# Kernel optimization log

Measured on AMD Instinct MI355X. Metric: run time of the kernel, lower is better.

The kernel has to match this reference:

```python
import jax, jax.numpy as jnp
import numpy as np

D_MODEL = 1024
D_STATE = 16
D_CONV = 4
EXPAND = 2
D_INNER = EXPAND * D_MODEL          # 2048
DT_RANK = (D_MODEL + 15) // 16      # 64
B_SZ, L = 2, 2048


def setup_inputs() -> dict:
    key = jax.random.key(0)
    ks = jax.random.split(key, 14)
    s = 0.02
    dt_init = jax.random.uniform(ks[10], (D_INNER,), minval=1e-3, maxval=0.1)
    A = jnp.tile(jnp.arange(1, D_STATE + 1, dtype=jnp.float32)[None, :], (D_INNER, 1))
    return {
        "x_f": jax.random.normal(ks[0], (B_SZ, L, D_MODEL), jnp.float32),
        "x_h": jax.random.normal(ks[1], (B_SZ, L, D_MODEL), jnp.float32),
        "W_hf": s * jax.random.normal(ks[2], (D_MODEL, D_MODEL), jnp.float32),
        "b_hf": jnp.zeros((D_MODEL,), jnp.float32),
        "W_in": s * jax.random.normal(ks[3], (2 * D_INNER, D_MODEL), jnp.float32),
        "conv_w": s * jax.random.normal(ks[4], (D_INNER, 1, D_CONV), jnp.float32),
        "conv_b": jnp.zeros((D_INNER,), jnp.float32),
        "W_x": s * jax.random.normal(ks[5], (DT_RANK + 2 * D_STATE, D_INNER), jnp.float32),
        "W_dt": (DT_RANK ** -0.5) * jax.random.normal(ks[6], (D_INNER, DT_RANK), jnp.float32),
        "b_dt": jnp.log(jnp.expm1(dt_init)),
        "A_log": jnp.log(A),
        "D": jnp.ones((D_INNER,), jnp.float32),
        "W_out": s * jax.random.normal(ks[7], (D_MODEL, D_INNER), jnp.float32),
    }


def _mamba(x, W_in, conv_w, conv_b, W_x, W_dt, b_dt, A_log, D, W_out):
    B, Lx, _ = x.shape
    # in_proj -> x, z branches  [B, L, 2*d_inner]
    xz = jnp.einsum("bld,ed->ble", x, W_in)
    x_in, z = jnp.split(xz, 2, axis=-1)
    # causal depthwise conv1d, kernel d_conv, groups = d_inner
    x_nch = jnp.transpose(x_in, (0, 2, 1))  # [B, d_inner, L]
    x_conv = jax.lax.conv_general_dilated(
        x_nch, conv_w, window_strides=(1,), padding=[(D_CONV - 1, 0)],
        dimension_numbers=("NCH", "OIH", "NCH"), feature_group_count=D_INNER)
    x_c = jax.nn.silu(jnp.transpose(x_conv, (0, 2, 1)) + conv_b)  # [B, L, d_inner]
    # input-dependent dt, B, C
    x_dbl = jnp.einsum("ble,fe->blf", x_c, W_x)
    dt_r = x_dbl[..., :DT_RANK]
    B_ssm = x_dbl[..., DT_RANK:DT_RANK + D_STATE]          # [B, L, d_state]
    C_ssm = x_dbl[..., DT_RANK + D_STATE:]                  # [B, L, d_state]
    dt = jax.nn.softplus(jnp.einsum("blr,er->ble", dt_r, W_dt) + b_dt)  # [B, L, d_inner]
    A = -jnp.exp(A_log)  # [d_inner, d_state]

    # selective scan over time; carry h: [B, d_inner, d_state]
    def step(h, inp):
        dt_t, B_t, C_t, x_t = inp  # [B,d_inner], [B,d_state], [B,d_state], [B,d_inner]
        dA = jnp.exp(dt_t[:, :, None] * A)                       # [B, d_inner, d_state]
        dBx = dt_t[:, :, None] * B_t[:, None, :] * x_t[:, :, None]
        h = dA * h + dBx
        y_t = jnp.einsum("bes,bs->be", h, C_t)
        return h, y_t

    seq = (jnp.transpose(dt, (1, 0, 2)), jnp.transpose(B_ssm, (1, 0, 2)),
           jnp.transpose(C_ssm, (1, 0, 2)), jnp.transpose(x_c, (1, 0, 2)))
    h0 = jnp.zeros((B, D_INNER, D_STATE), x.dtype)
    _, ys = jax.lax.scan(step, h0, seq)
    y = jnp.transpose(ys, (1, 0, 2)) + D * x_c   # skip term
    y = y * jax.nn.silu(z)                        # output gate
    return jnp.einsum("ble,de->bld", y, W_out)


def reference(x_f, x_h, W_hf, b_hf, W_in, conv_w, conv_b, W_x, W_dt, b_dt, A_log, D, W_out):
    hf_gate = jax.nn.sigmoid(jnp.einsum("bld,ed->ble", x_h, W_hf) + b_hf)
    modulated = x_f * hf_gate
    return _mamba(modulated, W_in, conv_w, conv_b, W_x, W_dt, b_dt, A_log, D, W_out)
```

## Files before the change

### kernel.cpp

```cpp
#include <hip/hip_runtime.h>
#include <hip/hip_bf16.h>
#include <math.h>

#define L_SEQ  2048
#define BATCH  2
#define DMODEL 1024
#define DINNER 2048
#define DSTATE 16
#define NCHUNK 64
#define LCH    (L_SEQ / NCHUNK)

typedef __attribute__((ext_vector_type(8))) short bf16x8;
typedef __attribute__((ext_vector_type(4))) float f32x4;

__device__ __forceinline__ unsigned short f2bu(float x) {
    __hip_bfloat16 h = __float2bfloat16(x);
    return __builtin_bit_cast(unsigned short, h);
}
__device__ __forceinline__ float bu2f(unsigned short u) {
    __hip_bfloat16 h = __builtin_bit_cast(__hip_bfloat16, u);
    return __bfloat162float(h);
}
__device__ __forceinline__ float fast_exp2(float x) {
    float r; asm("v_exp_f32 %0, %1" : "=v"(r) : "v"(x)); return r;
}
#define LOG2E 1.44269504088896f

__global__ __launch_bounds__(256) void cvt_all(
    const float* __restrict__ Wout, const float* __restrict__ Win,
    const float* __restrict__ xh,   const float* __restrict__ Whf,
    const float* __restrict__ Wx,   const float* __restrict__ Wdt,
    __hip_bfloat16* __restrict__ dWout, __hip_bfloat16* __restrict__ dWin,
    __hip_bfloat16* __restrict__ dxh,   __hip_bfloat16* __restrict__ dWhf,
    __hip_bfloat16* __restrict__ dWx,   __hip_bfloat16* __restrict__ dWdt)
{
    int bid = blockIdx.x;
    const float* s; __hip_bfloat16* d;
    if (bid < 2048)       { s = Wout; d = dWout; }
    else if (bid < 6144)  { s = Win;  d = dWin;  bid -= 2048; }
    else if (bid < 10240) { s = xh;   d = dxh;   bid -= 6144; }
    else if (bid < 11264) { s = Whf;  d = dWhf;  bid -= 10240; }
    else if (bid < 11520) {
        bid -= 11264;
        const int i = (bid * 256 + threadIdx.x) * 4;
        const int r = i >> 11;
        ushort4 u = {0, 0, 0, 0};
        if (r < 96) {
            const float4 v = *reinterpret_cast<const float4*>(&Wx[i]);
            u.x = f2bu(v.x); u.y = f2bu(v.y); u.z = f2bu(v.z); u.w = f2bu(v.w);
        }
        *reinterpret_cast<ushort4*>(&dWx[i]) = u;
        return;
    }
    else                  { s = Wdt;  d = dWdt;  bid -= 11520; }
    const int i = (bid * 256 + threadIdx.x) * 4;
    const float4 v = *reinterpret_cast<const float4*>(&s[i]);
    ushort4 u;
    u.x = f2bu(v.x); u.y = f2bu(v.y); u.z = f2bu(v.z); u.w = f2bu(v.w);
    *reinterpret_cast<ushort4*>(&d[i]) = u;
}

__global__ __launch_bounds__(512) void mfma_gemm256(
    const __hip_bfloat16* __restrict__ A,
    const __hip_bfloat16* __restrict__ Bw,
    __hip_bfloat16* __restrict__ Cb,
    __hip_bfloat16* __restrict__ Cb2)
{
    __shared__ unsigned short As[2][256 * 64];
    __shared__ unsigned short Bs[2][256 * 64];
    const int tid = threadIdx.x;
    const int row0 = blockIdx.y * 256;
    const int col0 = blockIdx.x * 256;
    const int wid = tid >> 6, lane = tid & 63;
    const int wr = wid >> 2, wc = wid & 3;
    const int fr = lane & 15, fq = lane >> 4;

    f32x4 acc[8][4];
#pragma unroll
    for (int m = 0; m < 8; m++)
#pragma unroll
        for (int n = 0; n < 4; n++) acc[m][n] = (f32x4){0.f, 0.f, 0.f, 0.f};

    size_t gA[4], gB[4];
    int ld0[4];
#pragma unroll
    for (int l = 0; l < 4; l++) {
        const int item = l * 512 + tid;
        const int r = item >> 3, sl = item & 7;
        gA[l] = (size_t)(row0 + r) * 1024 + sl * 8;
        gB[l] = (size_t)(col0 + r) * 1024 + sl * 8;
        ld0[l] = item * 8;
    }

#if __has_builtin(__builtin_amdgcn_global_load_lds)
    auto STAGE = [&](int buf, int koff) {
#pragma unroll
        for (int l = 0; l < 4; l++)
            __builtin_amdgcn_global_load_lds(
                (const __attribute__((address_space(1))) unsigned int*)(A + gA[l] + koff),
                (__attribute__((address_space(3))) unsigned int*)&As[buf][ld0[l]], 16, 0, 0);
#pragma unroll
        for (int l = 0; l < 4; l++)
            __builtin_amdgcn_global_load_lds(
                (const __attribute__((address_space(1))) unsigned int*)(Bw + gB[l] + koff),
                (__attribute__((address_space(3))) unsigned int*)&Bs[buf][ld0[l]], 16, 0, 0);
    };
#else
    auto STAGE = [&](int buf, int koff) {
#pragma unroll
        for (int l = 0; l < 4; l++) {
            *reinterpret_cast<uint4*>(&As[buf][ld0[l]]) =
                *reinterpret_cast<const uint4*>(A + gA[l] + koff);
            *reinterpret_cast<uint4*>(&Bs[buf][ld0[l]]) =
                *reinterpret_cast<const uint4*>(Bw + gB[l] + koff);
        }
    };
#endif

    STAGE(0, 0);
    __syncthreads();
    int buf = 0;
    for (int t = 0; t < 16; t++) {
        if (t + 1 < 16) STAGE(buf ^ 1, (t + 1) * 64);
#pragma unroll
        for (int ks = 0; ks < 2; ks++) {
            bf16x8 a[8], b[4];
#pragma unroll
            for (int m = 0; m < 8; m++)
                a[m] = *reinterpret_cast<const bf16x8*>(
                    &As[buf][(wr * 128 + m * 16 + fr) * 64 + ks * 32 + fq * 8]);
#pragma unroll
            for (int n = 0; n < 4; n++)
                b[n] = *reinterpret_cast<const bf16x8*>(
                    &Bs[buf][(wc * 64 + n * 16 + fr) * 64 + ks * 32 + fq * 8]);
#pragma unroll
            for (int m = 0; m < 8; m++)
#pragma unroll
                for (int n = 0; n < 4; n++)
                    acc[m][n] = __builtin_amdgcn_mfma_f32_16x16x32_bf16(
                        a[m], b[n], acc[m][n], 0, 0, 0);
        }
        __syncthreads();
        buf ^= 1;
    }

    const int r0 = row0 + wr * 128;
    const int c0 = col0 + wc * 64;
    const bool isx = (col0 < 2048);
#pragma unroll
    for (int m = 0; m < 8; m++)
#pragma unroll
        for (int n = 0; n < 4; n++) {
            const int col = c0 + n * 16 + fr;
#pragma unroll
            for (int j = 0; j < 4; j++) {
                const int row = r0 + m * 16 + fq * 4 + j;
                const __hip_bfloat16 v = __float2bfloat16(acc[m][n][j]);
                if (isx) Cb[(size_t)row * 2048 + col] = v;
                else     Cb2[(size_t)row * 2048 + col - 2048] = v;
            }
        }
}

template <int EPI>
__global__ __launch_bounds__(256) void mfma_gemm(
    const __hip_bfloat16* __restrict__ A, int lda,
    const __hip_bfloat16* __restrict__ Bw, int ldb,
    int ksz,
    float* __restrict__ Cf, int ldc,
    __hip_bfloat16* __restrict__ Cb,
    const float* __restrict__ bias,
    const float* __restrict__ mul, int ldmul)
{
    __shared__ unsigned short As[128 * 32];
    __shared__ unsigned short Bs[128 * 32];
    const int tid = threadIdx.x;
    const int row0 = blockIdx.y * 128;
    const int col0 = blockIdx.x * 128;
    const int wid = tid >> 6, lane = tid & 63;
    const int wr = wid >> 1, wc = wid & 1;
    const int fr = lane & 15, fq = lane >> 4;
    const int kz0 = blockIdx.z * ksz;

    f32x4 acc[4][4];
#pragma unroll
    for (int i = 0; i < 4; i++)
#pragma unroll
        for (int j = 0; j < 4; j++) acc[i][j] = (f32x4){0.f, 0.f, 0.f, 0.f};

    const int i0 = tid, i1 = tid + 256;
    const size_t ga0 = (size_t)(row0 + (i0 >> 2)) * lda + (i0 & 3) * 8;
    const size_t ga1 = (size_t)(row0 + (i1 >> 2)) * lda + (i1 & 3) * 8;
    const size_t gb0 = (size_t)(col0 + (i0 >> 2)) * ldb + (i0 & 3) * 8;
    const size_t gb1 = (size_t)(col0 + (i1 >> 2)) * ldb + (i1 & 3) * 8;
    const int nk = ksz >> 5;

    for (int kk = 0; kk < nk; kk++) {
        const int koff = kz0 + kk * 32;
#if __has_builtin(__builtin_amdgcn_global_load_lds)
        __syncthreads();
        __builtin_amdgcn_global_load_lds(
            (const __attribute__((address_space(1))) unsigned int*)(A + ga0 + koff),
            (__attribute__((address_space(3))) unsigned int*)&As[i0 * 8], 16, 0, 0);
        __builtin_amdgcn_global_load_lds(
            (const __attribute__((address_space(1))) unsigned int*)(A + ga1 + koff),
            (__attribute__((address_space(3))) unsigned int*)&As[i1 * 8], 16, 0, 0);
        __builtin_amdgcn_global_load_lds(
            (const __attribute__((address_space(1))) unsigned int*)(Bw + gb0 + koff),
            (__attribute__((address_space(3))) unsigned int*)&Bs[i0 * 8], 16, 0, 0);
        __builtin_amdgcn_global_load_lds(
            (const __attribute__((address_space(1))) unsigned int*)(Bw + gb1 + koff),
            (__attribute__((address_space(3))) unsigned int*)&Bs[i1 * 8], 16, 0, 0);
        __syncthreads();
#else
        const uint4 va0 = *reinterpret_cast<const uint4*>(A + ga0 + koff);
        const uint4 va1 = *reinterpret_cast<const uint4*>(A + ga1 + koff);
        const uint4 vb0 = *reinterpret_cast<const uint4*>(Bw + gb0 + koff);
        const uint4 vb1 = *reinterpret_cast<const uint4*>(Bw + gb1 + koff);
        __syncthreads();
        *reinterpret_cast<uint4*>(&As[i0 * 8]) = va0;
        *reinterpret_cast<uint4*>(&As[i1 * 8]) = va1;
        *reinterpret_cast<uint4*>(&Bs[i0 * 8]) = vb0;
        *reinterpret_cast<uint4*>(&Bs[i1 * 8]) = vb1;
        __syncthreads();
#endif
        bf16x8 af[4], bq[4];
#pragma unroll
        for (int rb = 0; rb < 4; rb++)
            af[rb] = *reinterpret_cast<const bf16x8*>(
                &As[(wr * 64 + rb * 16 + fr) * 32 + fq * 8]);
#pragma unroll
        for (int cb = 0; cb < 4; cb++)
            bq[cb] = *reinterpret_cast<const bf16x8*>(
                &Bs[(wc * 64 + cb * 16 + fr) * 32 + fq * 8]);
#pragma unroll
        for (int rb = 0; rb < 4; rb++)
#pragma unroll
            for (int cb = 0; cb < 4; cb++)
                acc[rb][cb] = __builtin_amdgcn_mfma_f32_16x16x32_bf16(
                    af[rb], bq[cb], acc[rb][cb], 0, 0, 0);
    }

    float* Cz = Cf;
    if (EPI == 0)
        Cz = Cf + (size_t)blockIdx.z * (size_t)(gridDim.y * 128) * ldc;
    const int r0 = row0 + wr * 64, c0 = col0 + wc * 64;
#pragma unroll
    for (int rb = 0; rb < 4; rb++)
#pragma unroll
        for (int cb = 0; cb < 4; cb++) {
            const int col = c0 + cb * 16 + fr;
#pragma unroll
            for (int j = 0; j < 4; j++) {
                const int row = r0 + rb * 16 + fq * 4 + j;
                float v = acc[rb][cb][j];
                if (EPI == 0) {
                    Cz[(size_t)row * ldc + col] = v;
                } else if (EPI == 1) {
                    v = 1.f / (1.f + __expf(-(v + bias[col])));
                    v *= mul[(size_t)row * ldmul + col];
                    Cb[(size_t)row * ldc + col] = __float2bfloat16(v);
                } else {
                    v += bias[col];
                    v = (v > 20.f) ? v : log1pf(__expf(v));
                    Cb[(size_t)row * ldc + col] = __float2bfloat16(v);
                }
            }
        }
}

__global__ __launch_bounds__(256) void reduce_xdbl(
    const float* __restrict__ part, float* __restrict__ xdbl,
    __hip_bfloat16* __restrict__ dtr)
{
    const int i = blockIdx.x * 256 + threadIdx.x;
    float s = 0.f;
#pragma unroll
    for (int j = 0; j < 8; j++) s += part[(size_t)j * 524288 + i];
    xdbl[i] = s;
    const int col = i & 127;
    if (col < 64) dtr[((i >> 7) << 6) + col] = __float2bfloat16(s);
}

__global__ __launch_bounds__(256) void conv_silu_kernel(
    const __hip_bfloat16* __restrict__ xin_b, const float* __restrict__ cw,
    const float* __restrict__ cb, __hip_bfloat16* __restrict__ xcb)
{
    int gid = blockIdx.x * 256 + threadIdx.x;
    int e = gid & (DINNER - 1);
    int row = gid >> 11;
    int t = row & (L_SEQ - 1);
    float s = cb[e];
#pragma unroll
    for (int j = 0; j < 4; j++) {
        int tt = t - 3 + j;
        if (tt >= 0)
            s = fmaf(cw[e * 4 + j],
                     __bfloat162float(xin_b[(size_t)(row - 3 + j) * 2048 + e]), s);
    }
    xcb[(size_t)row * 2048 + e] = __float2bfloat16(s / (1.f + __expf(-s)));
}

__global__ __launch_bounds__(256) void scan_pass_a(
    const __hip_bfloat16* __restrict__ dtb, const __hip_bfloat16* __restrict__ xcb,
    const float* __restrict__ xdbl, const float* __restrict__ A_log,
    __hip_bfloat16* __restrict__ hloc, __hip_bfloat16* __restrict__ Pp)
{
    __shared__ float sB[LCH][16];
    const int tid = threadIdx.x;
    const int e = (blockIdx.x << 8) + tid;
    const int chunk = blockIdx.y;
    const int b = blockIdx.z;
    const int t0 = chunk * LCH;

    if (tid < LCH * 4) {
        const int r = tid >> 2, sl = tid & 3;
        *(float4*)&sB[r][sl * 4] =
            *(const float4*)&xdbl[(size_t)(b * L_SEQ + t0 + r) * 128 + 64 + sl * 4];
    }
    float av[16];
#pragma unroll
    for (int sq = 0; sq < 4; sq++) {
        const float4 al = *(const float4*)&A_log[e * 16 + sq * 4];
#pragma unroll
        for (int j = 0; j < 4; j++)
            av[sq * 4 + j] = -fast_exp2(((const float*)&al)[j] * LOG2E);
    }
    float h[16];
#pragma unroll
    for (int s = 0; s < 16; s++) h[s] = 0.f;
    float sdt = 0.f;
    __syncthreads();

    const size_t rb = (size_t)(b * L_SEQ + t0) * 2048 + e;
    float dtv_n = __bfloat162float(dtb[rb]);
    float xv_n = __bfloat162float(xcb[rb]);
    for (int t = 0; t < LCH; t++) {
        const float dtv = dtv_n, xv = xv_n;
        if (t + 1 < LCH) {
            dtv_n = __bfloat162float(dtb[rb + (size_t)(t + 1) * 2048]);
            xv_n = __bfloat162float(xcb[rb + (size_t)(t + 1) * 2048]);
        }
        sdt += dtv;
        const float dtx = dtv * xv;
        const float dl2 = dtv * LOG2E;
#pragma unroll
        for (int sq = 0; sq < 4; sq++) {
            const float4 B4 = *(const float4*)&sB[t][sq * 4];
#pragma unroll
            for (int j = 0; j < 4; j++) {
                const int s = sq * 4 + j;
                const float Bv = ((const float*)&B4)[j];
                h[s] = fmaf(fast_exp2(dl2 * av[s]), h[s], Bv * dtx);
            }
        }
    }
    const size_t o = (((size_t)chunk * BATCH + b) * 2048 + e) * 16;
#pragma unroll
    for (int sq = 0; sq < 4; sq++) {
        ushort4 uh, up;
        uh.x = f2bu(h[sq * 4]);     uh.y = f2bu(h[sq * 4 + 1]);
        uh.z = f2bu(h[sq * 4 + 2]); uh.w = f2bu(h[sq * 4 + 3]);
        up.x = f2bu(fast_exp2(av[sq * 4] * sdt * LOG2E));
        up.y = f2bu(fast_exp2(av[sq * 4 + 1] * sdt * LOG2E));
        up.z = f2bu(fast_exp2(av[sq * 4 + 2] * sdt * LOG2E));
        up.w = f2bu(fast_exp2(av[sq * 4 + 3] * sdt * LOG2E));
        *(ushort4*)&hloc[o + sq * 4] = uh;
        *(ushort4*)&Pp[o + sq * 4] = up;
    }
}

__global__ __launch_bounds__(256) void scan_pass_b(
    const __hip_bfloat16* __restrict__ hloc, const __hip_bfloat16* __restrict__ Pp,
    __hip_bfloat16* __restrict__ h0)
{
    const int idx = blockIdx.x * 256 + threadIdx.x;
    float h = 0.f;
    h0[idx] = __float2bfloat16(0.f);
    for (int c = 0; c < NCHUNK - 1; c++) {
        const float P = __bfloat162float(Pp[(size_t)c * 65536 + idx]);
        const float hl = __bfloat162float(hloc[(size_t)c * 65536 + idx]);
        h = fmaf(P, h, hl);
        h0[(size_t)(c + 1) * 65536 + idx] = __float2bfloat16(h);
    }
}

__global__ __launch_bounds__(256) void scan_pass_c(
    const __hip_bfloat16* __restrict__ dtb, const __hip_bfloat16* __restrict__ xcb,
    const float* __restrict__ xdbl, const __hip_bfloat16* __restrict__ zb,
    const float* __restrict__ A_log, const float* __restrict__ Dw,
    const __hip_bfloat16* __restrict__ h0, __hip_bfloat16* __restrict__ yb)
{
    __shared__ float sB[LCH][16];
    __shared__ float sC[LCH][16];
    const int tid = threadIdx.x;
    const int e = (blockIdx.x << 8) + tid;
    const int chunk = blockIdx.y;
    const int b = blockIdx.z;
    const int t0 = chunk * LCH;

    if (tid < LCH * 4) {
        const int r = tid >> 2, sl = tid & 3;
        *(float4*)&sB[r][sl * 4] =
            *(const float4*)&xdbl[(size_t)(b * L_SEQ + t0 + r) * 128 + 64 + sl * 4];
    } else if (tid < LCH * 8) {
        const int t2 = tid - LCH * 4;
        const int r = t2 >> 2, sl = t2 & 3;
        *(float4*)&sC[r][sl * 4] =
            *(const float4*)&xdbl[(size_t)(b * L_SEQ + t0 + r) * 128 + 80 + sl * 4];
    }
    float av[16];
#pragma unroll
    for (int sq = 0; sq < 4; sq++) {
        const float4 al = *(const float4*)&A_log[e * 16 + sq * 4];
#pragma unroll
        for (int j = 0; j < 4; j++)
            av[sq * 4 + j] = -fast_exp2(((const float*)&al)[j] * LOG2E);
    }
    const float De = Dw[e];
    float h[16];
    const size_t o = (((size_t)chunk * BATCH + b) * 2048 + e) * 16;
#pragma unroll
    for (int sq = 0; sq < 4; sq++) {
        const ushort4 hv = *(const ushort4*)&h0[o + sq * 4];
        h[sq * 4]     = bu2f(hv.x); h[sq * 4 + 1] = bu2f(hv.y);
        h[sq * 4 + 2] = bu2f(hv.z); h[sq * 4 + 3] = bu2f(hv.w);
    }
    __syncthreads();

    const size_t rb = (size_t)(b * L_SEQ + t0) * 2048 + e;
    float dtv_n = __bfloat162float(dtb[rb]);
    float xv_n = __bfloat162float(xcb[rb]);
    float zv_n = __bfloat162float(zb[rb]);
    for (int t = 0; t < LCH; t++) {
        const float dtv = dtv_n, xv = xv_n, zv = zv_n;
        if (t + 1 < LCH) {
            dtv_n = __bfloat162float(dtb[rb + (size_t)(t + 1) * 2048]);
            xv_n = __bfloat162float(xcb[rb + (size_t)(t + 1) * 2048]);
            zv_n = __bfloat162float(zb[rb + (size_t)(t + 1) * 2048]);
        }
        const float dtx = dtv * xv;
        const float dl2 = dtv * LOG2E;
        float yp0 = 0.f, yp1 = 0.f, yp2 = 0.f, yp3 = 0.f;
#pragma unroll
        for (int sq = 0; sq < 4; sq++) {
            const float4 B4 = *(const float4*)&sB[t][sq * 4];
            const float4 C4 = *(const float4*)&sC[t][sq * 4];
#pragma unroll
            for (int j = 0; j < 4; j++) {
                const int s = sq * 4 + j;
                const float Bv = ((const float*)&B4)[j];
                const float Cv = ((const float*)&C4)[j];
                h[s] = fmaf(fast_exp2(dl2 * av[s]), h[s], Bv * dtx);
                if (sq == 0) yp0 = fmaf(h[s], Cv, yp0);
                else if (sq == 1) yp1 = fmaf(h[s], Cv, yp1);
                else if (sq == 2) yp2 = fmaf(h[s], Cv, yp2);
                else yp3 = fmaf(h[s], Cv, yp3);
            }
        }
        float yv = (yp0 + yp1) + (yp2 + yp3);
        yv = fmaf(De, xv, yv);
        const float sig = 1.f / (1.f + __expf(-zv));
        yb[rb + (size_t)t * 2048] = __float2bfloat16(yv * zv * sig);
    }
}

extern "C" void kernel_launch(void* const* d_in, const int* in_sizes, int n_in,
                              void* d_out, int out_size, void* d_ws, size_t ws_size,
                              hipStream_t stream)
{
    const float* x_f    = (const float*)d_in[0];
    const float* x_h    = (const float*)d_in[1];
    const float* W_hf   = (const float*)d_in[2];
    const float* b_hf   = (const float*)d_in[3];
    const float* W_in   = (const float*)d_in[4];
    const float* conv_w = (const float*)d_in[5];
    const float* conv_b = (const float*)d_in[6];
    const float* W_x    = (const float*)d_in[7];
    const float* W_dt   = (const float*)d_in[8];
    const float* b_dt   = (const float*)d_in[9];
    const float* A_log  = (const float*)d_in[10];
    const float* Dw     = (const float*)d_in[11];
    const float* W_out  = (const float*)d_in[12];
    float* out = (float*)d_out;
    float* ws  = (float*)d_ws;

    __hip_bfloat16* wout_b = (__hip_bfloat16*)(ws);
    __hip_bfloat16* win_b  = (__hip_bfloat16*)(ws + 1048576);
    __hip_bfloat16* xh_b   = (__hip_bfloat16*)(ws + 3145728);
    __hip_bfloat16* whf_b  = (__hip_bfloat16*)(ws + 5242880);
    __hip_bfloat16* m_b    = (__hip_bfloat16*)(ws + 5767168);
    __hip_bfloat16* hloc   = (__hip_bfloat16*)(ws + 1048576);
    __hip_bfloat16* Pp     = (__hip_bfloat16*)(ws + 3145728);
    __hip_bfloat16* h0     = (__hip_bfloat16*)(ws + 5242880);
    __hip_bfloat16* wx_b   = (__hip_bfloat16*)(ws + 7864320);
    __hip_bfloat16* wdt_b  = (__hip_bfloat16*)(ws + 7995392);
    __hip_bfloat16* dtr_b  = (__hip_bfloat16*)(ws + 8060928);
    float*          xdbl   = ws + 10289152;
    __hip_bfloat16* xin_b  = (__hip_bfloat16*)(ws + 10813440);
    __hip_bfloat16* z_b    = (__hip_bfloat16*)(ws + 15007744);
    __hip_bfloat16* xc_b   = (__hip_bfloat16*)(ws + 19202048);
    float*          part   = ws + 23396352;
    __hip_bfloat16* dt_b   = (__hip_bfloat16*)(ws + 27590656);
    __hip_bfloat16* yb     = (__hip_bfloat16*)(ws + 31784960);

    cvt_all<<<11648, 256, 0, stream>>>(
        W_out, W_in, x_h, W_hf, W_x, W_dt,
        wout_b, win_b, xh_b, whf_b, wx_b, wdt_b);

    mfma_gemm<1><<<dim3(8, 32, 1), 256, 0, stream>>>(
        xh_b, DMODEL, whf_b, DMODEL, DMODEL,
        nullptr, DMODEL, m_b, b_hf, x_f, DMODEL);

    mfma_gemm256<<<dim3(16, 16, 1), 512, 0, stream>>>(
        m_b, win_b, xin_b, z_b);

    conv_silu_kernel<<<32768, 256, 0, stream>>>(
        xin_b, conv_w, conv_b, xc_b);

    mfma_gemm<0><<<dim3(1, 32, 8), 256, 0, stream>>>(
        xc_b, DINNER, wx_b, DINNER, 256,
        part, 128, nullptr, nullptr, nullptr, 0);
    reduce_xdbl<<<2048, 256, 0, stream>>>(part, xdbl, dtr_b);

    mfma_gemm<3><<<dim3(16, 32, 1), 256, 0, stream>>>(
        dtr_b, 64, wdt_b, 64, 64,
        nullptr, 2048, dt_b, b_dt, nullptr, 0);

    scan_pass_a<<<dim3(8, NCHUNK - 1, BATCH), 256, 0, stream>>>(
        dt_b, xc_b, xdbl, A_log, hloc, Pp);
    scan_pass_b<<<256, 256, 0, stream>>>(hloc, Pp, h0);
    scan_pass_c<<<dim3(8, NCHUNK, BATCH), 256, 0, stream>>>(
        dt_b, xc_b, xdbl, z_b, A_log, Dw, h0, yb);

    mfma_gemm<0><<<dim3(8, 32, 1), 256, 0, stream>>>(
        yb, DINNER, wout_b, DINNER, DINNER,
        out, DMODEL, nullptr, nullptr, nullptr, 0);
}
```

Baseline: 300.5 us.

## Split-K the output projection and swap block order for weight reuse

The final W_out GEMM (4096x1024, K=2048) now uses split-K with two slices into a float partial buffer. A new vectorized reduce kernel then sums the slices into the output. This doubles the block count from 256 so more of the GPU's compute units are busy. A SWAP template flag also swaps the grid axes for the hf-gate GEMM and the output GEMM, so consecutive blocks share a weight column tile, which may improve L2 reuse. The cost is an extra kernel launch plus a write and read of two 16 MB fp32 partial buffers.

New measurement: 289.1 us. -3.8%, faster.

```diff
diff --git a/kernel.cpp b/kernel.cpp
--- a/kernel.cpp
+++ b/kernel.cpp
@@ -162,7 +162,7 @@
         }
 }
 
-template <int EPI>
+template <int EPI, bool SWAP>
 __global__ __launch_bounds__(256) void mfma_gemm(
     const __hip_bfloat16* __restrict__ A, int lda,
     const __hip_bfloat16* __restrict__ Bw, int ldb,
@@ -175,8 +175,10 @@
     __shared__ unsigned short As[128 * 32];
     __shared__ unsigned short Bs[128 * 32];
     const int tid = threadIdx.x;
-    const int row0 = blockIdx.y * 128;
-    const int col0 = blockIdx.x * 128;
+    const int by = SWAP ? blockIdx.x : blockIdx.y;
+    const int bx = SWAP ? blockIdx.y : blockIdx.x;
+    const int row0 = by * 128;
+    const int col0 = bx * 128;
     const int wid = tid >> 6, lane = tid & 63;
     const int wr = wid >> 1, wc = wid & 1;
     const int fr = lane & 15, fq = lane >> 4;
@@ -242,8 +244,10 @@
     }
 
     float* Cz = Cf;
-    if (EPI == 0)
-        Cz = Cf + (size_t)blockIdx.z * (size_t)(gridDim.y * 128) * ldc;
+    if (EPI == 0) {
+        const int nrows = (SWAP ? gridDim.x : gridDim.y) * 128;
+        Cz = Cf + (size_t)blockIdx.z * (size_t)nrows * ldc;
+    }
     const int r0 = row0 + wr * 64, c0 = col0 + wc * 64;
 #pragma unroll
     for (int rb = 0; rb < 4; rb++)
@@ -280,6 +284,16 @@
     xdbl[i] = s;
     const int col = i & 127;
     if (col < 64) dtr[((i >> 7) << 6) + col] = __float2bfloat16(s);
+}
+
+__global__ __launch_bounds__(256) void reduce_out(
+    const float* __restrict__ part, float* __restrict__ out)
+{
+    const int i = (blockIdx.x * 256 + threadIdx.x) * 4;
+    const float4 a = *reinterpret_cast<const float4*>(&part[i]);
+    const float4 b = *reinterpret_cast<const float4*>(&part[4194304 + i]);
+    *reinterpret_cast<float4*>(&out[i]) =
+        make_float4(a.x + b.x, a.y + b.y, a.z + b.z, a.w + b.w);
 }
 
 __global__ __launch_bounds__(256) void conv_silu_kernel(
@@ -502,13 +516,14 @@
     __hip_bfloat16* xc_b   = (__hip_bfloat16*)(ws + 19202048);
     float*          part   = ws + 23396352;
     __hip_bfloat16* dt_b   = (__hip_bfloat16*)(ws + 27590656);
+    float*          part7  = ws + 23396352;
     __hip_bfloat16* yb     = (__hip_bfloat16*)(ws + 31784960);
 
     cvt_all<<<11648, 256, 0, stream>>>(
         W_out, W_in, x_h, W_hf, W_x, W_dt,
         wout_b, win_b, xh_b, whf_b, wx_b, wdt_b);
 
-    mfma_gemm<1><<<dim3(8, 32, 1), 256, 0, stream>>>(
+    mfma_gemm<1, true><<<dim3(32, 8, 1), 256, 0, stream>>>(
         xh_b, DMODEL, whf_b, DMODEL, DMODEL,
         nullptr, DMODEL, m_b, b_hf, x_f, DMODEL);
 
@@ -518,12 +533,12 @@
     conv_silu_kernel<<<32768, 256, 0, stream>>>(
         xin_b, conv_w, conv_b, xc_b);
 
-    mfma_gemm<0><<<dim3(1, 32, 8), 256, 0, stream>>>(
+    mfma_gemm<0, false><<<dim3(1, 32, 8), 256, 0, stream>>>(
         xc_b, DINNER, wx_b, DINNER, 256,
         part, 128, nullptr, nullptr, nullptr, 0);
     reduce_xdbl<<<2048, 256, 0, stream>>>(part, xdbl, dtr_b);
 
-    mfma_gemm<3><<<dim3(16, 32, 1), 256, 0, stream>>>(
+    mfma_gemm<3, false><<<dim3(16, 32, 1), 256, 0, stream>>>(
         dtr_b, 64, wdt_b, 64, 64,
         nullptr, 2048, dt_b, b_dt, nullptr, 0);
 
@@ -533,7 +548,8 @@
     scan_pass_c<<<dim3(8, NCHUNK, BATCH), 256, 0, stream>>>(
         dt_b, xc_b, xdbl, z_b, A_log, Dw, h0, yb);
 
-    mfma_gemm<0><<<dim3(8, 32, 1), 256, 0, stream>>>(
-        yb, DINNER, wout_b, DINNER, DINNER,
-        out, DMODEL, nullptr, nullptr, nullptr, 0);
-}
+    mfma_gemm<0, true><<<dim3(32, 8, 2), 256, 0, stream>>>(
+        yb, DINNER, wout_b, DINNER, DINNER / 2,
+        part7, DMODEL, nullptr, nullptr, nullptr, 0);
+    reduce_out<<<4096, 256, 0, stream>>>(part7, out);
+}
```
